# Performance work log

Hardware: AMD Instinct MI355X
Metric: run time of the kernel (lower is better)

The kernel has to match this reference:

```python
import jax, jax.numpy as jnp
import numpy as np

N_NODES = 100000
N_EDGES = 600000
IN_CH = 128
HID = 128


def setup_inputs() -> dict:
    key = jax.random.key(0)
    ks = jax.random.split(key, 8)
    x = jax.random.normal(ks[0], (N_NODES, IN_CH), dtype=jnp.float32)
    edge_index = jax.random.randint(ks[1], (2, N_EDGES), 0, N_NODES, dtype=jnp.int64)
    # Linear weights stored as (in, out); scaled like torch default init
    W1 = jax.random.normal(ks[2], (2 * IN_CH, HID), dtype=jnp.float32) / np.sqrt(2 * IN_CH)
    b1 = jnp.zeros((HID,), dtype=jnp.float32)
    W2 = jax.random.normal(ks[3], (HID, HID), dtype=jnp.float32) / np.sqrt(HID)
    b2 = jnp.zeros((HID,), dtype=jnp.float32)
    W3 = jax.random.normal(ks[4], (HID, 1), dtype=jnp.float32) / np.sqrt(HID)
    b3 = jnp.zeros((1,), dtype=jnp.float32)
    return {"x": x, "edge_index": edge_index, "W1": W1, "b1": b1,
            "W2": W2, "b2": b2, "W3": W3, "b3": b3}


def reference(x, edge_index, W1, b1, W2, b2, W3, b3):
    src = edge_index[0]
    tgt = edge_index[1]
    # gather + concat: [n_edges, 2*in_channels]
    h = jnp.concatenate([x[src, :], x[tgt, :]], axis=1)
    h = jax.nn.elu(h @ W1 + b1)
    h = jax.nn.elu(h @ W2 + b2)
    h = h @ W3 + b3  # [n_edges, 1]
    return jnp.squeeze(h)  # squeeze=True path -> [n_edges]
```

## Files before the change

### kernel.cpp

```cpp
#include <hip/hip_runtime.h>

#define N_NODES 100000
#define N_EDGES 600000
#define NT2 9375
#define LDW 264
typedef _Float16 f16x8 __attribute__((ext_vector_type(8)));
typedef __attribute__((ext_vector_type(4))) float f32x4;

__device__ __forceinline__ float elu_f(float v) {
    return v > 0.0f ? v : (__expf(v) - 1.0f);
}

extern "C" __global__ __launch_bounds__(256)
void k0_convert(const float* __restrict__ x, _Float16* __restrict__ xh) {
    const int step = gridDim.x * blockDim.x;
    for (int c = blockIdx.x * blockDim.x + threadIdx.x; c < (N_NODES * 128) / 8;
         c += step) {
        const float4 a0 = *(const float4*)(x + (size_t)c * 8);
        const float4 a1 = *(const float4*)(x + (size_t)c * 8 + 4);
        f16x8 h;
        h[0] = (_Float16)a0.x; h[1] = (_Float16)a0.y;
        h[2] = (_Float16)a0.z; h[3] = (_Float16)a0.w;
        h[4] = (_Float16)a1.x; h[5] = (_Float16)a1.y;
        h[6] = (_Float16)a1.z; h[7] = (_Float16)a1.w;
        *(f16x8*)(xh + (size_t)c * 8) = h;
    }
}

extern "C" __global__ __launch_bounds__(256, 2)
void k2_edge_mlp(const _Float16* __restrict__ xh, const void* __restrict__ eiv,
                 const float* __restrict__ W1, const float* __restrict__ b1,
                 const float* __restrict__ W2, const float* __restrict__ b2,
                 const float* __restrict__ W3, const float* __restrict__ b3,
                 float* __restrict__ out) {
    __shared__ __align__(16) _Float16 sRaw[2][64 * LDW];
    __shared__ float sPart[2][4][64];
    __shared__ int sFlag;

    const int t = threadIdx.x;
    const int w = t >> 6, lane = t & 63;
    const int ln = lane & 15, kg = lane >> 4;
    const int row_s = t >> 2;
    const int qb = (t & 3) * 32;
    const float b3v = b3[0];
    const int stride = gridDim.x;

    if (t < 64) {
        unsigned v = ((const unsigned*)eiv)[2 * t + 1];
        unsigned long long bm = __ballot(v == 0u);
        if (t == 0) sFlag = (bm == ~0ull) ? 1 : 0;
    }

    f16x8 bf1[2][2][4];
#pragma unroll
    for (int half = 0; half < 2; ++half)
#pragma unroll
        for (int c = 0; c < 2; ++c) {
            const int n = w * 32 + c * 16 + ln;
#pragma unroll
            for (int ks = 0; ks < 4; ++ks) {
                f16x8 v;
#pragma unroll
                for (int j = 0; j < 8; ++j) {
                    int k = half * 128 + ks * 32 + kg * 8 + j;
                    v[j] = (_Float16)W1[k * 128 + n];
                }
                bf1[half][c][ks] = v;
            }
        }

    f16x8 bf2[2][4];
#pragma unroll
    for (int c = 0; c < 2; ++c) {
        const int n = w * 32 + c * 16 + ln;
#pragma unroll
        for (int ks = 0; ks < 4; ++ks) {
            f16x8 v;
#pragma unroll
            for (int j = 0; j < 8; ++j) {
                int k = ks * 32 + kg * 8 + j;
                v[j] = (_Float16)W2[k * 128 + n];
            }
            bf2[c][ks] = v;
        }
    }

    float b1v[2], b2v[2], w3v[2];
#pragma unroll
    for (int c = 0; c < 2; ++c) {
        int col = w * 32 + c * 16 + ln;
        b1v[c] = b1[col]; b2v[c] = b2[col]; w3v[c] = W3[col];
    }

    __syncthreads();
    const int mode64 = sFlag;
    const int tile0 = blockIdx.x;

    int se_nx, ge_nx;
    {
        int e = tile0 * 64 + row_s;
        int se, ge;
        if (mode64) {
            se = (int)((const long long*)eiv)[e];
            ge = (int)((const long long*)eiv)[N_EDGES + e];
        } else {
            se = ((const int*)eiv)[e];
            ge = ((const int*)eiv)[N_EDGES + e];
        }
        const _Float16* pa = xh + (size_t)se * 128 + qb;
        const _Float16* pb = xh + (size_t)ge * 128 + qb;
#pragma unroll
        for (int i = 0; i < 4; ++i) {
            f16x8 ga = *(const f16x8*)(pa + i * 8);
            f16x8 gb = *(const f16x8*)(pb + i * 8);
            *(f16x8*)(&sRaw[0][row_s * LDW + qb + i * 8]) = ga;
            *(f16x8*)(&sRaw[0][row_s * LDW + 128 + qb + i * 8]) = gb;
        }
    }
    {
        int t1 = tile0 + stride;
        int t1c = (t1 < NT2) ? t1 : tile0;
        int e = t1c * 64 + row_s;
        if (mode64) {
            se_nx = (int)((const long long*)eiv)[e];
            ge_nx = (int)((const long long*)eiv)[N_EDGES + e];
        } else {
            se_nx = ((const int*)eiv)[e];
            ge_nx = ((const int*)eiv)[N_EDGES + e];
        }
    }
    __syncthreads();

    int p = 0;
    int prevE0 = -1;
    for (int tile = tile0; tile < NT2; tile += stride) {
        const int nt = tile + stride;
        const int ntc = (nt < NT2) ? nt : tile;

        const _Float16* pa = xh + (size_t)se_nx * 128 + qb;
        const _Float16* pb = xh + (size_t)ge_nx * 128 + qb;
        f16x8 Ga[4], Gb[4];
#pragma unroll
        for (int i = 0; i < 4; ++i) {
            Ga[i] = *(const f16x8*)(pa + i * 8);
            Gb[i] = *(const f16x8*)(pb + i * 8);
        }

        {
            int n2 = nt + stride;
            int n2c = (n2 < NT2) ? n2 : ntc;
            int e = n2c * 64 + row_s;
            if (mode64) {
                se_nx = (int)((const long long*)eiv)[e];
                ge_nx = (int)((const long long*)eiv)[N_EDGES + e];
            } else {
                se_nx = ((const int*)eiv)[e];
                ge_nx = ((const int*)eiv)[N_EDGES + e];
            }
        }

        if (prevE0 >= 0 && t < 64)
            out[prevE0 + t] = sPart[p ^ 1][0][t] + sPart[p ^ 1][1][t] +
                              sPart[p ^ 1][2][t] + sPart[p ^ 1][3][t] + b3v;

        f32x4 acc1[4][2];
#pragma unroll
        for (int rt = 0; rt < 4; ++rt)
#pragma unroll
            for (int c = 0; c < 2; ++c) acc1[rt][c] = (f32x4){0.f, 0.f, 0.f, 0.f};

#pragma unroll
        for (int ks = 0; ks < 4; ++ks) {
#pragma unroll
            for (int rt = 0; rt < 4; ++rt) {
                f16x8 a_s = *(const f16x8*)(&sRaw[p][(rt * 16 + ln) * LDW + ks * 32 + kg * 8]);
                f16x8 a_t = *(const f16x8*)(&sRaw[p][(rt * 16 + ln) * LDW + 128 + ks * 32 + kg * 8]);
#pragma unroll
                for (int c = 0; c < 2; ++c) {
                    acc1[rt][c] = __builtin_amdgcn_mfma_f32_16x16x32_f16(
                        a_s, bf1[0][c][ks], acc1[rt][c], 0, 0, 0);
                    acc1[rt][c] = __builtin_amdgcn_mfma_f32_16x16x32_f16(
                        a_t, bf1[1][c][ks], acc1[rt][c], 0, 0, 0);
                }
            }
        }
        __syncthreads();

#pragma unroll
        for (int rt = 0; rt < 4; ++rt)
#pragma unroll
            for (int c = 0; c < 2; ++c) {
                const int col = w * 32 + c * 16 + ln;
#pragma unroll
                for (int reg = 0; reg < 4; ++reg) {
                    const int row = rt * 16 + kg * 4 + reg;
                    sRaw[p][row * LDW + col] =
                        (_Float16)elu_f(acc1[rt][c][reg] + b1v[c]);
                }
            }
        __syncthreads();

        f32x4 acc2[4][2];
#pragma unroll
        for (int rt = 0; rt < 4; ++rt)
#pragma unroll
            for (int c = 0; c < 2; ++c) acc2[rt][c] = (f32x4){0.f, 0.f, 0.f, 0.f};

#pragma unroll
        for (int ks = 0; ks < 4; ++ks) {
#pragma unroll
            for (int rt = 0; rt < 4; ++rt) {
                f16x8 a = *(const f16x8*)(&sRaw[p][(rt * 16 + ln) * LDW + ks * 32 + kg * 8]);
#pragma unroll
                for (int c = 0; c < 2; ++c)
                    acc2[rt][c] = __builtin_amdgcn_mfma_f32_16x16x32_f16(
                        a, bf2[c][ks], acc2[rt][c], 0, 0, 0);
            }
        }

#pragma unroll
        for (int rt = 0; rt < 4; ++rt) {
            float pr[4] = {0.f, 0.f, 0.f, 0.f};
#pragma unroll
            for (int c = 0; c < 2; ++c) {
#pragma unroll
                for (int reg = 0; reg < 4; ++reg)
                    pr[reg] += elu_f(acc2[rt][c][reg] + b2v[c]) * w3v[c];
            }
#pragma unroll
            for (int m = 1; m < 16; m <<= 1)
#pragma unroll
                for (int reg = 0; reg < 4; ++reg) pr[reg] += __shfl_xor(pr[reg], m, 64);
            if (ln == 0) {
#pragma unroll
                for (int reg = 0; reg < 4; ++reg)
                    sPart[p][w][rt * 16 + kg * 4 + reg] = pr[reg];
            }
        }

#pragma unroll
        for (int i = 0; i < 4; ++i) {
            *(f16x8*)(&sRaw[p ^ 1][row_s * LDW + qb + i * 8]) = Ga[i];
            *(f16x8*)(&sRaw[p ^ 1][row_s * LDW + 128 + qb + i * 8]) = Gb[i];
        }

        prevE0 = tile * 64;
        __syncthreads();
        p ^= 1;
    }

    if (prevE0 >= 0 && t < 64)
        out[prevE0 + t] = sPart[p ^ 1][0][t] + sPart[p ^ 1][1][t] +
                          sPart[p ^ 1][2][t] + sPart[p ^ 1][3][t] + b3v;
}

extern "C" void kernel_launch(void* const* d_in, const int* in_sizes, int n_in,
                              void* d_out, int out_size, void* d_ws, size_t ws_size,
                              hipStream_t stream) {
    const float* x  = (const float*)d_in[0];
    const void*  ei = d_in[1];
    const float* W1 = (const float*)d_in[2];
    const float* b1 = (const float*)d_in[3];
    const float* W2 = (const float*)d_in[4];
    const float* b2 = (const float*)d_in[5];
    const float* W3 = (const float*)d_in[6];
    const float* b3 = (const float*)d_in[7];
    float* out = (float*)d_out;

    _Float16* xh = (_Float16*)((char*)d_ws + 256);

    k0_convert<<<2048, 256, 0, stream>>>(x, xh);
    k2_edge_mlp<<<512, 256, 0, stream>>>(xh, ei, W1, b1, W2, b2, W3, b3, out);
}
```

Before: 207.3 us.

## Shrink LDS to a single raw buffer plus H1 buffer to fit three blocks per CU

Replaces the double-buffered 64x264 raw tile with one raw buffer and a separate 64x136 H1 buffer. The next tile's gathered rows are written into the raw buffer right after layer-1 MMAs finish, and the per-iteration barriers drop from three to two. Launch bounds go to 3 blocks per CU and the grid grows to 768 blocks. LDS per block falls from about 67KB to about 51KB, which allows three blocks per CU for more latency hiding. The cost is tighter register pressure under the higher occupancy bound.

```diff
diff --git a/kernel.cpp b/kernel.cpp
--- a/kernel.cpp
+++ b/kernel.cpp
@@ -4,6 +4,7 @@
 #define N_EDGES 600000
 #define NT2 9375
 #define LDW 264
+#define LDH 136
 typedef _Float16 f16x8 __attribute__((ext_vector_type(8)));
 typedef __attribute__((ext_vector_type(4))) float f32x4;
 
@@ -27,14 +28,15 @@
     }
 }
 
-extern "C" __global__ __launch_bounds__(256, 2)
+extern "C" __global__ __launch_bounds__(256, 3)
 void k2_edge_mlp(const _Float16* __restrict__ xh, const void* __restrict__ eiv,
                  const float* __restrict__ W1, const float* __restrict__ b1,
                  const float* __restrict__ W2, const float* __restrict__ b2,
                  const float* __restrict__ W3, const float* __restrict__ b3,
                  float* __restrict__ out) {
-    __shared__ __align__(16) _Float16 sRaw[2][64 * LDW];
-    __shared__ float sPart[2][4][64];
+    __shared__ __align__(16) _Float16 sRaw[64 * LDW];
+    __shared__ __align__(16) _Float16 sH1[64 * LDH];
+    __shared__ float sPart[4][64];
     __shared__ int sFlag;
 
     const int t = threadIdx.x;
@@ -113,8 +115,8 @@
         for (int i = 0; i < 4; ++i) {
             f16x8 ga = *(const f16x8*)(pa + i * 8);
             f16x8 gb = *(const f16x8*)(pb + i * 8);
-            *(f16x8*)(&sRaw[0][row_s * LDW + qb + i * 8]) = ga;
-            *(f16x8*)(&sRaw[0][row_s * LDW + 128 + qb + i * 8]) = gb;
+            *(f16x8*)(&sRaw[row_s * LDW + qb + i * 8]) = ga;
+            *(f16x8*)(&sRaw[row_s * LDW + 128 + qb + i * 8]) = gb;
         }
     }
     {
@@ -131,7 +133,6 @@
     }
     __syncthreads();
 
-    int p = 0;
     int prevE0 = -1;
     for (int tile = tile0; tile < NT2; tile += stride) {
         const int nt = tile + stride;
@@ -159,10 +160,6 @@
             }
         }
 
-        if (prevE0 >= 0 && t < 64)
-            out[prevE0 + t] = sPart[p ^ 1][0][t] + sPart[p ^ 1][1][t] +
-                              sPart[p ^ 1][2][t] + sPart[p ^ 1][3][t] + b3v;
-
         f32x4 acc1[4][2];
 #pragma unroll
         for (int rt = 0; rt < 4; ++rt)
@@ -173,8 +170,8 @@
         for (int ks = 0; ks < 4; ++ks) {
 #pragma unroll
             for (int rt = 0; rt < 4; ++rt) {
-                f16x8 a_s = *(const f16x8*)(&sRaw[p][(rt * 16 + ln) * LDW + ks * 32 + kg * 8]);
-                f16x8 a_t = *(const f16x8*)(&sRaw[p][(rt * 16 + ln) * LDW + 128 + ks * 32 + kg * 8]);
+                f16x8 a_s = *(const f16x8*)(&sRaw[(rt * 16 + ln) * LDW + ks * 32 + kg * 8]);
+                f16x8 a_t = *(const f16x8*)(&sRaw[(rt * 16 + ln) * LDW + 128 + ks * 32 + kg * 8]);
 #pragma unroll
                 for (int c = 0; c < 2; ++c) {
                     acc1[rt][c] = __builtin_amdgcn_mfma_f32_16x16x32_f16(
@@ -186,6 +183,10 @@
         }
         __syncthreads();
 
+        if (prevE0 >= 0 && t < 64)
+            out[prevE0 + t] = sPart[0][t] + sPart[1][t] +
+                              sPart[2][t] + sPart[3][t] + b3v;
+
 #pragma unroll
         for (int rt = 0; rt < 4; ++rt)
 #pragma unroll
@@ -194,10 +195,16 @@
 #pragma unroll
                 for (int reg = 0; reg < 4; ++reg) {
                     const int row = rt * 16 + kg * 4 + reg;
-                    sRaw[p][row * LDW + col] =
+                    sH1[row * LDH + col] =
                         (_Float16)elu_f(acc1[rt][c][reg] + b1v[c]);
                 }
             }
+
+#pragma unroll
+        for (int i = 0; i < 4; ++i) {
+            *(f16x8*)(&sRaw[row_s * LDW + qb + i * 8]) = Ga[i];
+            *(f16x8*)(&sRaw[row_s * LDW + 128 + qb + i * 8]) = Gb[i];
+        }
         __syncthreads();
 
         f32x4 acc2[4][2];
@@ -210,7 +217,7 @@
         for (int ks = 0; ks < 4; ++ks) {
 #pragma unroll
             for (int rt = 0; rt < 4; ++rt) {
-                f16x8 a = *(const f16x8*)(&sRaw[p][(rt * 16 + ln) * LDW + ks * 32 + kg * 8]);
+                f16x8 a = *(const f16x8*)(&sH1[(rt * 16 + ln) * LDH + ks * 32 + kg * 8]);
 #pragma unroll
                 for (int c = 0; c < 2; ++c)
                     acc2[rt][c] = __builtin_amdgcn_mfma_f32_16x16x32_f16(
@@ -234,24 +241,17 @@
             if (ln == 0) {
 #pragma unroll
                 for (int reg = 0; reg < 4; ++reg)
-                    sPart[p][w][rt * 16 + kg * 4 + reg] = pr[reg];
-            }
-        }
-
-#pragma unroll
-        for (int i = 0; i < 4; ++i) {
-            *(f16x8*)(&sRaw[p ^ 1][row_s * LDW + qb + i * 8]) = Ga[i];
-            *(f16x8*)(&sRaw[p ^ 1][row_s * LDW + 128 + qb + i * 8]) = Gb[i];
+                    sPart[w][rt * 16 + kg * 4 + reg] = pr[reg];
+            }
         }
 
         prevE0 = tile * 64;
-        __syncthreads();
-        p ^= 1;
-    }
-
+    }
+
+    __syncthreads();
     if (prevE0 >= 0 && t < 64)
-        out[prevE0 + t] = sPart[p ^ 1][0][t] + sPart[p ^ 1][1][t] +
-                          sPart[p ^ 1][2][t] + sPart[p ^ 1][3][t] + b3v;
+        out[prevE0 + t] = sPart[0][t] + sPart[1][t] +
+                          sPart[2][t] + sPart[3][t] + b3v;
 }
 
 extern "C" void kernel_launch(void* const* d_in, const int* in_sizes, int n_in,
@@ -270,5 +270,5 @@
     _Float16* xh = (_Float16*)((char*)d_ws + 256);
 
     k0_convert<<<2048, 256, 0, stream>>>(x, xh);
-    k2_edge_mlp<<<512, 256, 0, stream>>>(xh, ei, W1, b1, W2, b2, W3, b3, out);
-}
+    k2_edge_mlp<<<768, 256, 0, stream>>>(xh, ei, W1, b1, W2, b2, W3, b3, out);
+}
```

Result: slower. 298.0 us (+43.7%).
